# Kernel optimization log

Measured on AMD Instinct MI355X. Metric: run time of the kernel, lower is better.

The kernel has to match this reference:

```python
import jax, jax.numpy as jnp
import numpy as np

H = 12
DH = 64
SCALE = DH ** -0.5

def _ln(x, g, b):
    m = jnp.mean(x, axis=-1, keepdims=True)
    v = jnp.mean((x - m) ** 2, axis=-1, keepdims=True)
    return (x - m) / jnp.sqrt(v + 1e-5) * g + b

def _heads(t):
    b, n, _ = t.shape
    return t.reshape(b, n, H, DH).transpose(0, 2, 1, 3)

def _merge(t):
    b, h, n, d = t.shape
    return t.transpose(0, 2, 1, 3).reshape(b, n, h * d)

def _attn_zero(q, k, v):
    # zero-attn sink: one all-zero K/V token appended -> extra logit exactly 0
    dots = jnp.einsum('bhid,bhjd->bhij', q, k) * SCALE
    dots = jnp.pad(dots, ((0, 0), (0, 0), (0, 0), (0, 1)))
    a = jax.nn.softmax(dots, axis=-1)[..., :-1]  # zero V row contributes nothing
    return jnp.einsum('bhij,bhjd->bhid', a, v)

def _ffn(x, w1, b1, w2, b2):
    return jax.nn.gelu(x @ w1 + b1, approximate=False) @ w2 + b2

def _forward(img, clinic, ln1_g, ln1_b, w_qkv, w_o, b_o, ln2_g, ln2_b,
             w_ff1, b_ff1, w_ff2, b_ff2,
             cn_i_g, cn_i_b, cn_c_g, cn_c_b,
             w_iq, w_ik, w_iv, w_cq, w_ck, w_cv,
             w_io, b_io, w_co, b_co,
             fn_i_g, fn_i_b, fn_c_g, fn_c_b,
             iff_w1, iff_b1, iff_w2, iff_b2,
             cff_w1, cff_b1, cff_w2, cff_b2):
    L = ln1_g.shape[0]
    for l in range(L):  # PreNorm self-attention Transformer stack on image tokens
        xn = _ln(img, ln1_g[l], ln1_b[l])
        q, k, v = jnp.split(xn @ w_qkv[l], 3, axis=-1)
        out = _merge(_attn_zero(_heads(q), _heads(k), _heads(v))) @ w_o[l] + b_o[l]
        img = img + out
        xn = _ln(img, ln2_g[l], ln2_b[l])
        img = img + _ffn(xn, w_ff1[l], b_ff1[l], w_ff2[l], b_ff2[l])
    # Transformer_Cross: dual-stream cross + self attention fusion
    i_n = _ln(img, cn_i_g, cn_i_b)
    c_n = _ln(clinic, cn_c_g, cn_c_b)
    iq, ik, iv = _heads(i_n @ w_iq), _heads(i_n @ w_ik), _heads(i_n @ w_iv)
    cq, ck, cv = _heads(c_n @ w_cq), _heads(c_n @ w_ck), _heads(c_n @ w_cv)
    i_out = (_attn_zero(iq, ck, cv) + _attn_zero(iq, ik, iv)) * 0.5
    c_out = (_attn_zero(cq, ik, iv) + _attn_zero(cq, ck, cv)) * 0.5
    img = img + (_merge(i_out) @ w_io + b_io)
    clinic = clinic + (_merge(c_out) @ w_co + b_co)
    img = img + _ffn(_ln(img, fn_i_g, fn_i_b), iff_w1, iff_b1, iff_w2, iff_b2)
    clinic = clinic + _ffn(_ln(clinic, fn_c_g, fn_c_b), cff_w1, cff_b1, cff_w2, cff_b2)
    return img, clinic

def setup_inputs() -> dict:
    B, NI, NC, D, M, L = 4, 1024, 256, 768, 3072, 2
    INNER = H * DH
    keys = iter(jax.random.split(jax.random.key(0), 48))
    def rn(shape, s=0.02):
        return jax.random.normal(next(keys), shape, jnp.float32) * s
    return {
        'img': jax.random.normal(next(keys), (B, NI, D), jnp.float32),
        'clinic': jax.random.normal(next(keys), (B, NC, D), jnp.float32),
        'ln1_g': jnp.ones((L, D), jnp.float32), 'ln1_b': jnp.zeros((L, D), jnp.float32),
        'w_qkv': rn((L, D, 3 * INNER)), 'w_o': rn((L, INNER, D)), 'b_o': jnp.zeros((L, D), jnp.float32),
        'ln2_g': jnp.ones((L, D), jnp.float32), 'ln2_b': jnp.zeros((L, D), jnp.float32),
        'w_ff1': rn((L, D, M)), 'b_ff1': jnp.zeros((L, M), jnp.float32),
        'w_ff2': rn((L, M, D)), 'b_ff2': jnp.zeros((L, D), jnp.float32),
        'cn_i_g': jnp.ones((D,), jnp.float32), 'cn_i_b': jnp.zeros((D,), jnp.float32),
        'cn_c_g': jnp.ones((D,), jnp.float32), 'cn_c_b': jnp.zeros((D,), jnp.float32),
        'w_iq': rn((D, INNER)), 'w_ik': rn((D, INNER)), 'w_iv': rn((D, INNER)),
        'w_cq': rn((D, INNER)), 'w_ck': rn((D, INNER)), 'w_cv': rn((D, INNER)),
        'w_io': rn((INNER, D)), 'b_io': jnp.zeros((D,), jnp.float32),
        'w_co': rn((INNER, D)), 'b_co': jnp.zeros((D,), jnp.float32),
        'fn_i_g': jnp.ones((D,), jnp.float32), 'fn_i_b': jnp.zeros((D,), jnp.float32),
        'fn_c_g': jnp.ones((D,), jnp.float32), 'fn_c_b': jnp.zeros((D,), jnp.float32),
        'iff_w1': rn((D, M)), 'iff_b1': jnp.zeros((M,), jnp.float32),
        'iff_w2': rn((M, D)), 'iff_b2': jnp.zeros((D,), jnp.float32),
        'cff_w1': rn((D, M)), 'cff_b1': jnp.zeros((M,), jnp.float32),
        'cff_w2': rn((M, D)), 'cff_b2': jnp.zeros((D,), jnp.float32),
    }

def reference(img, clinic, ln1_g, ln1_b, w_qkv, w_o, b_o, ln2_g, ln2_b,
              w_ff1, b_ff1, w_ff2, b_ff2,
              cn_i_g, cn_i_b, cn_c_g, cn_c_b,
              w_iq, w_ik, w_iv, w_cq, w_ck, w_cv,
              w_io, b_io, w_co, b_co,
              fn_i_g, fn_i_b, fn_c_g, fn_c_b,
              iff_w1, iff_b1, iff_w2, iff_b2,
              cff_w1, cff_b1, cff_w2, cff_b2):
    return _forward(img, clinic, ln1_g, ln1_b, w_qkv, w_o, b_o, ln2_g, ln2_b,
                    w_ff1, b_ff1, w_ff2, b_ff2,
                    cn_i_g, cn_i_b, cn_c_g, cn_c_b,
                    w_iq, w_ik, w_iv, w_cq, w_ck, w_cv,
                    w_io, b_io, w_co, b_co,
                    fn_i_g, fn_i_b, fn_c_g, fn_c_b,
                    iff_w1, iff_b1, iff_w2, iff_b2,
                    cff_w1, cff_b1, cff_w2, cff_b2)
```

## Files before the change

kernel.cpp:

```cpp
#include <hip/hip_runtime.h>
#include <stdint.h>
#include <math.h>

typedef unsigned short u16;
typedef short  s16x8 __attribute__((ext_vector_type(8)));
typedef float  f32x4 __attribute__((ext_vector_type(4)));

#define DEVI __device__ __forceinline__

DEVI float b2f(u16 u){ union{unsigned int i; float f;} v; v.i = ((unsigned int)u)<<16; return v.f; }
DEVI u16 f2b(float f){
  union{float f; unsigned int i;} v; v.f = f;
  unsigned int r = v.i + 0x7FFFu + ((v.i >> 16) & 1u);
  return (u16)(r >> 16);
}

template<int MODE, int SPLITK>
__launch_bounds__(256, 2)
__global__ void gemm_bt(const u16* __restrict__ A, const u16* __restrict__ Bt,
                        const float* __restrict__ bias, u16* __restrict__ outb,
                        float* __restrict__ resid, int M, int N, int K)
{
  __shared__ __align__(16) u16 lds_a[128*32];
  __shared__ __align__(16) u16 lds_b[128*32];
  const int tid = threadIdx.x;
  const int w = tid >> 6, l = tid & 63;
  const int q = l >> 4, r = l & 15;
  const int wm = w & 1, wn = w >> 1;
  const size_t m0 = (size_t)blockIdx.y * 128, n0 = (size_t)blockIdx.x * 128;
  const int kslice = K / SPLITK;
  const int kbeg = (SPLITK > 1) ? (int)blockIdx.z * kslice : 0;

  const int srow = tid >> 2;
  const int scol = (tid & 3) * 8;
  const u16* pa0 = A  + (m0 + srow)      * (size_t)K + kbeg + scol;
  const u16* pa1 = A  + (m0 + 64 + srow) * (size_t)K + kbeg + scol;
  const u16* pb0 = Bt + (n0 + srow)      * (size_t)K + kbeg + scol;
  const u16* pb1 = Bt + (n0 + 64 + srow) * (size_t)K + kbeg + scol;

  f32x4 acc[4][4];
  f32x4 zero = {0.f, 0.f, 0.f, 0.f};
#pragma unroll
  for (int i = 0; i < 4; i++)
#pragma unroll
    for (int j = 0; j < 4; j++) acc[i][j] = zero;

  auto compute = [&]() {
    s16x8 af[4], bfr[4];
#pragma unroll
    for (int mm = 0; mm < 4; mm++)
      af[mm] = *(const s16x8*)&lds_a[(wm*64 + mm*16 + r)*32 + q*8];
#pragma unroll
    for (int nn = 0; nn < 4; nn++)
      bfr[nn] = *(const s16x8*)&lds_b[(wn*64 + nn*16 + r)*32 + q*8];
#pragma unroll
    for (int mm = 0; mm < 4; mm++)
#pragma unroll
      for (int nn = 0; nn < 4; nn++)
        acc[mm][nn] = __builtin_amdgcn_mfma_f32_16x16x32_bf16(af[mm], bfr[nn], acc[mm][nn], 0, 0, 0);
  };

  s16x8 a0_0 = *(const s16x8*)(pa0);
  s16x8 a1_0 = *(const s16x8*)(pa1);
  s16x8 b0_0 = *(const s16x8*)(pb0);
  s16x8 b1_0 = *(const s16x8*)(pb1);
  s16x8 a0_1 = *(const s16x8*)(pa0 + 32);
  s16x8 a1_1 = *(const s16x8*)(pa1 + 32);
  s16x8 b0_1 = *(const s16x8*)(pb0 + 32);
  s16x8 b1_1 = *(const s16x8*)(pb1 + 32);

  const int niter = kslice / 32;
  for (int it = 0; it < niter; it += 2){
    __syncthreads();
    *(s16x8*)&lds_a[srow*32 + scol]        = a0_0;
    *(s16x8*)&lds_a[(64 + srow)*32 + scol] = a1_0;
    *(s16x8*)&lds_b[srow*32 + scol]        = b0_0;
    *(s16x8*)&lds_b[(64 + srow)*32 + scol] = b1_0;
    __syncthreads();
    if (it + 2 < niter){
      int k2 = (it + 2) * 32;
      a0_0 = *(const s16x8*)(pa0 + k2);
      a1_0 = *(const s16x8*)(pa1 + k2);
      b0_0 = *(const s16x8*)(pb0 + k2);
      b1_0 = *(const s16x8*)(pb1 + k2);
    }
    compute();
    __syncthreads();
    *(s16x8*)&lds_a[srow*32 + scol]        = a0_1;
    *(s16x8*)&lds_a[(64 + srow)*32 + scol] = a1_1;
    *(s16x8*)&lds_b[srow*32 + scol]        = b0_1;
    *(s16x8*)&lds_b[(64 + srow)*32 + scol] = b1_1;
    __syncthreads();
    if (it + 3 < niter){
      int k3 = (it + 3) * 32;
      a0_1 = *(const s16x8*)(pa0 + k3);
      a1_1 = *(const s16x8*)(pa1 + k3);
      b0_1 = *(const s16x8*)(pb0 + k3);
      b1_1 = *(const s16x8*)(pb1 + k3);
    }
    compute();
  }

#pragma unroll
  for (int nn = 0; nn < 4; nn++){
    size_t col = n0 + wn*64 + nn*16 + r;
    float bv = 0.0f;
    if (MODE != 0 && (SPLITK == 1 || blockIdx.z == 0)) bv = bias[col];
#pragma unroll
    for (int mm = 0; mm < 4; mm++){
#pragma unroll
      for (int j = 0; j < 4; j++){
        size_t row = m0 + wm*64 + mm*16 + q*4 + j;
        float v = acc[mm][nn][j] + bv;
        if (MODE == 1) v = 0.5f * v * (1.0f + erff(v * 0.70710678118654752f));
        if (MODE == 2){
          if (SPLITK > 1) atomicAdd(&resid[row * N + col], v);
          else            resid[row * N + col] += v;
        } else {
          outb[row * N + col] = f2b(v);
        }
      }
    }
  }
}

__launch_bounds__(256, 2)
__global__ void attn_zero_kernel(const u16* __restrict__ Qp, const u16* __restrict__ Kp,
                                 const u16* __restrict__ vT, u16* __restrict__ Op,
                                 int Nq, int Nkv, int LDq, int LDk,
                                 float outw, int accumulate)
{
  __shared__ __align__(16) u16 lds_k[32*64];
  __shared__ __align__(16) u16 lds_v[64*32];
  __shared__ __align__(16) u16 lds_p[4][16*40];

  const int tid = threadIdx.x;
  const int w = tid >> 6, l = tid & 63;
  const int q = l >> 4, r = l & 15;
  const int h = blockIdx.y, b = blockIdx.z;
  const int q0 = blockIdx.x * 64 + w * 16;

  s16x8 qf[2];
  {
    const u16* qrow = Qp + (size_t)(b*Nq + q0 + r) * LDq + h*64;
    qf[0] = *(const s16x8*)(qrow + q*8);
    qf[1] = *(const s16x8*)(qrow + 32 + q*8);
  }

  float m_[4], l_[4];
  f32x4 o[4];
  f32x4 zero = {0.f, 0.f, 0.f, 0.f};
#pragma unroll
  for (int j = 0; j < 4; j++){ m_[j] = 0.0f; l_[j] = 1.0f; }
#pragma unroll
  for (int nn = 0; nn < 4; nn++) o[nn] = zero;

  const u16* Kbase = Kp + (size_t)b * Nkv * LDk + h*64;
  const u16* gk = Kbase + (size_t)(tid >> 3) * LDk + (((tid & 7) ^ ((tid >> 3) & 7)) << 3);
  const u16* Vbase = vT + ((size_t)b * 768 + h*64) * (size_t)Nkv;
  const u16* gv = Vbase + (size_t)(tid >> 2) * Nkv + ((tid & 3) << 3);

  for (int kv0 = 0; kv0 < Nkv; kv0 += 32){
    s16x8 kvv = *(const s16x8*)(gk + (size_t)kv0 * LDk);
    s16x8 vvv = *(const s16x8*)(gv + kv0);
    __syncthreads();
    *(s16x8*)&lds_k[tid * 8] = kvv;
    *(s16x8*)&lds_v[tid * 8] = vvv;
    __syncthreads();

    f32x4 s[2];
#pragma unroll
    for (int kk = 0; kk < 2; kk++){
      int row = kk*16 + r;
      s16x8 kf0 = *(const s16x8*)&lds_k[row*64 + ((q       ^ (row & 7)) << 3)];
      s16x8 kf1 = *(const s16x8*)&lds_k[row*64 + (((4 + q) ^ (row & 7)) << 3)];
      f32x4 t = zero;
      t = __builtin_amdgcn_mfma_f32_16x16x32_bf16(qf[0], kf0, t, 0, 0, 0);
      t = __builtin_amdgcn_mfma_f32_16x16x32_bf16(qf[1], kf1, t, 0, 0, 0);
      s[kk] = t * 0.125f;
    }

    float p0[4], p1[4], al[4];
#pragma unroll
    for (int j = 0; j < 4; j++){
      float mx = fmaxf(s[0][j], s[1][j]);
#pragma unroll
      for (int d = 1; d < 16; d <<= 1) mx = fmaxf(mx, __shfl_xor(mx, d));
      float mn = fmaxf(m_[j], mx);
      float a  = __expf(m_[j] - mn);
      p0[j] = __expf(s[0][j] - mn);
      p1[j] = __expf(s[1][j] - mn);
      float rs = p0[j] + p1[j];
#pragma unroll
      for (int d = 1; d < 16; d <<= 1) rs += __shfl_xor(rs, d);
      l_[j] = l_[j] * a + rs;
      m_[j] = mn; al[j] = a;
    }
#pragma unroll
    for (int nn = 0; nn < 4; nn++){
      f32x4 t = o[nn];
#pragma unroll
      for (int j = 0; j < 4; j++) t[j] *= al[j];
      o[nn] = t;
    }

    u16* P = &lds_p[w][0];
#pragma unroll
    for (int j = 0; j < 4; j++){
      P[(q*4 + j)*40 + r]      = f2b(p0[j]);
      P[(q*4 + j)*40 + 16 + r] = f2b(p1[j]);
    }
    s16x8 pf = *(const s16x8*)&P[r*40 + q*8];
#pragma unroll
    for (int nn = 0; nn < 4; nn++){
      int row = nn*16 + r;
      s16x8 vf = *(const s16x8*)&lds_v[row*32 + (q << 3)];
      o[nn] = __builtin_amdgcn_mfma_f32_16x16x32_bf16(pf, vf, o[nn], 0, 0, 0);
    }
  }

#pragma unroll
  for (int j = 0; j < 4; j++){
    float inv = outw / l_[j];
    size_t rowoff = (size_t)(b*Nq + q0 + q*4 + j) * 768 + h*64;
#pragma unroll
    for (int nn = 0; nn < 4; nn++){
      float v = o[nn][j] * inv;
      size_t idx = rowoff + nn*16 + r;
      if (accumulate) v += b2f(Op[idx]);
      Op[idx] = f2b(v);
    }
  }
}

__launch_bounds__(256)
__global__ void ln_kernel(const float* __restrict__ x, const float* __restrict__ g,
                          const float* __restrict__ bta, u16* __restrict__ out)
{
  __shared__ float red[8];
  const size_t row = blockIdx.x;
  const float* xr = x + row * 768;
  int t = threadIdx.x;
  float v0 = xr[t], v1 = xr[t + 256], v2 = xr[t + 512];
  float s  = v0 + v1 + v2;
  float s2 = v0*v0 + v1*v1 + v2*v2;
#pragma unroll
  for (int d = 1; d < 64; d <<= 1){ s += __shfl_xor(s, d); s2 += __shfl_xor(s2, d); }
  int w = t >> 6;
  if ((t & 63) == 0){ red[w] = s; red[4 + w] = s2; }
  __syncthreads();
  s  = red[0] + red[1] + red[2] + red[3];
  s2 = red[4] + red[5] + red[6] + red[7];
  float mean = s * (1.0f / 768.0f);
  float var  = s2 * (1.0f / 768.0f) - mean * mean;
  float rstd = rsqrtf(var + 1e-5f);
  u16* orow = out + row * 768;
  orow[t]       = f2b((v0 - mean) * rstd * g[t]       + bta[t]);
  orow[t + 256] = f2b((v1 - mean) * rstd * g[t + 256] + bta[t + 256]);
  orow[t + 512] = f2b((v2 - mean) * rstd * g[t + 512] + bta[t + 512]);
}

__global__ void transpose_kernel(const float* __restrict__ in, u16* __restrict__ out, int R, int C)
{
  __shared__ u16 tile[64][65];
  int c0 = blockIdx.x * 64, r0 = blockIdx.y * 64;
  for (int i = threadIdx.y; i < 64; i += 4)
    tile[i][threadIdx.x] = f2b(in[(size_t)(r0 + i) * C + c0 + threadIdx.x]);
  __syncthreads();
  for (int i = threadIdx.y; i < 64; i += 4)
    out[(size_t)(c0 + i) * R + r0 + threadIdx.x] = tile[threadIdx.x][i];
}

__global__ void transpose_v_kernel(const u16* __restrict__ in, u16* __restrict__ out,
                                   int N, int LD, int coff)
{
  __shared__ u16 tile[64][65];
  int bz = blockIdx.z;
  int c0 = blockIdx.x * 64, n0 = blockIdx.y * 64;
  const u16* ib = in + ((size_t)bz * N + n0) * LD + coff + c0;
  for (int i = threadIdx.y; i < 64; i += 4)
    tile[i][threadIdx.x] = ib[(size_t)i * LD + threadIdx.x];
  __syncthreads();
  u16* ob = out + ((size_t)bz * 768 + c0) * N + n0;
  for (int i = threadIdx.y; i < 64; i += 4)
    ob[(size_t)i * N + threadIdx.x] = tile[threadIdx.x][i];
}

__global__ void copy_f32(const float* __restrict__ in, float* __restrict__ out, long n4){
  long i = (long)blockIdx.x * blockDim.x + threadIdx.x;
  long stride = (long)gridDim.x * blockDim.x;
  const f32x4* in4 = (const f32x4*)in;
  f32x4* out4 = (f32x4*)out;
  for (; i < n4; i += stride) out4[i] = in4[i];
}

extern "C" void kernel_launch(void* const* d_in, const int* in_sizes, int n_in,
                              void* d_out, int out_size, void* d_ws, size_t ws_size,
                              hipStream_t stream)
{
  const int B = 4, NI = 1024, NC = 256, D = 768, FF = 3072, H = 12, L = 2;
  const int RI = B * NI;
  const int RC = B * NC;

  const float* img    = (const float*)d_in[0];
  const float* clinic = (const float*)d_in[1];
  const float* ln1_g  = (const float*)d_in[2];
  const float* ln1_b  = (const float*)d_in[3];
  const float* w_qkv  = (const float*)d_in[4];
  const float* w_o    = (const float*)d_in[5];
  const float* b_o    = (const float*)d_in[6];
  const float* ln2_g  = (const float*)d_in[7];
  const float* ln2_b  = (const float*)d_in[8];
  const float* w_ff1  = (const float*)d_in[9];
  const float* b_ff1  = (const float*)d_in[10];
  const float* w_ff2  = (const float*)d_in[11];
  const float* b_ff2  = (const float*)d_in[12];
  const float* cn_i_g = (const float*)d_in[13];
  const float* cn_i_b = (const float*)d_in[14];
  const float* cn_c_g = (const float*)d_in[15];
  const float* cn_c_b = (const float*)d_in[16];
  const float* w_iq   = (const float*)d_in[17];
  const float* w_ik   = (const float*)d_in[18];
  const float* w_iv   = (const float*)d_in[19];
  const float* w_cq   = (const float*)d_in[20];
  const float* w_ck   = (const float*)d_in[21];
  const float* w_cv   = (const float*)d_in[22];
  const float* w_io   = (const float*)d_in[23];
  const float* b_io   = (const float*)d_in[24];
  const float* w_co   = (const float*)d_in[25];
  const float* b_co   = (const float*)d_in[26];
  const float* fn_i_g = (const float*)d_in[27];
  const float* fn_i_b = (const float*)d_in[28];
  const float* fn_c_g = (const float*)d_in[29];
  const float* fn_c_b = (const float*)d_in[30];
  const float* iff_w1 = (const float*)d_in[31];
  const float* iff_b1 = (const float*)d_in[32];
  const float* iff_w2 = (const float*)d_in[33];
  const float* iff_b2 = (const float*)d_in[34];
  const float* cff_w1 = (const float*)d_in[35];
  const float* cff_b1 = (const float*)d_in[36];
  const float* cff_w2 = (const float*)d_in[37];
  const float* cff_b2 = (const float*)d_in[38];

  char* ws = (char*)d_ws;
  size_t off = 0;
  auto alloc = [&](size_t elems, size_t esz) -> void* {
    void* p = ws + off;
    off += ((elems * esz) + 255) & ~(size_t)255;
    return p;
  };
  u16* wqkvT[2]; u16* woT[2]; u16* ff1T[2]; u16* ff2T[2];
  for (int i = 0; i < 2; i++) wqkvT[i] = (u16*)alloc((size_t)3*D*D, 2);
  for (int i = 0; i < 2; i++) woT[i]   = (u16*)alloc((size_t)D*D, 2);
  for (int i = 0; i < 2; i++) ff1T[i]  = (u16*)alloc((size_t)FF*D, 2);
  for (int i = 0; i < 2; i++) ff2T[i]  = (u16*)alloc((size_t)D*FF, 2);
  u16* wiqkvT = (u16*)alloc((size_t)3*D*D, 2);
  u16* wcqkvT = (u16*)alloc((size_t)3*D*D, 2);
  u16* wioT = (u16*)alloc((size_t)D*D, 2); u16* wcoT = (u16*)alloc((size_t)D*D, 2);
  u16* iff1T = (u16*)alloc((size_t)FF*D, 2); u16* iff2T = (u16*)alloc((size_t)D*FF, 2);
  u16* cff1T = (u16*)alloc((size_t)FF*D, 2); u16* cff2T = (u16*)alloc((size_t)D*FF, 2);

  float* img_f = (float*)alloc((size_t)RI*D, 4);
  float* cli_f = (float*)alloc((size_t)RC*D, 4);
  u16* xn_i = (u16*)alloc((size_t)RI*D, 2);
  u16* xn_c = (u16*)alloc((size_t)RC*D, 2);
  u16* region = (u16*)alloc((size_t)RI*FF, 2);
  u16* qkvb = region;
  u16* cqkv = region + (size_t)RI*3*D;
  u16* h1   = region;
  u16* ao_i = (u16*)alloc((size_t)RI*D, 2);
  u16* ao_c = (u16*)alloc((size_t)RC*D, 2);
  u16* vT_i = (u16*)alloc((size_t)B*D*NI, 2);
  u16* vT_c = (u16*)alloc((size_t)B*D*NC, 2);
  (void)ws_size; (void)in_sizes; (void)n_in; (void)out_size;

  auto T = [&](const float* in_, u16* out_, int R, int C){
    transpose_kernel<<<dim3(C/64, R/64), dim3(64, 4), 0, stream>>>(in_, out_, R, C);
  };
  auto TV = [&](const u16* in_, u16* out_, int N, int LD, int coff){
    transpose_v_kernel<<<dim3(D/64, N/64, B), dim3(64, 4), 0, stream>>>(in_, out_, N, LD, coff);
  };
  auto G0 = [&](const u16* A, const u16* Bt, u16* out_, int M, int N, int K){
    gemm_bt<0,1><<<dim3(N/128, M/128), 256, 0, stream>>>(A, Bt, nullptr, out_, nullptr, M, N, K);
  };
  auto G1 = [&](const u16* A, const u16* Bt, const float* bias, u16* out_, int M, int N, int K){
    gemm_bt<1,1><<<dim3(N/128, M/128), 256, 0, stream>>>(A, Bt, bias, out_, nullptr, M, N, K);
  };
  auto G2 = [&](const u16* A, const u16* Bt, const float* bias, float* resid, int M, int N, int K, int splitk){
    if (splitk == 4)
      gemm_bt<2,4><<<dim3(N/128, M/128, 4), 256, 0, stream>>>(A, Bt, bias, nullptr, resid, M, N, K);
    else if (splitk == 2)
      gemm_bt<2,2><<<dim3(N/128, M/128, 2), 256, 0, stream>>>(A, Bt, bias, nullptr, resid, M, N, K);
    else
      gemm_bt<2,1><<<dim3(N/128, M/128, 1), 256, 0, stream>>>(A, Bt, bias, nullptr, resid, M, N, K);
  };
  auto ATT = [&](const u16* Q, const u16* K_, const u16* vTp, u16* O,
                 int Nq, int Nkv, int LDq, int LDk, float w_, int acc_){
    attn_zero_kernel<<<dim3(Nq/64, H, B), 256, 0, stream>>>(Q, K_, vTp, O, Nq, Nkv, LDq, LDk, w_, acc_);
  };
  auto CP = [&](const float* in_, float* out_, long n){
    copy_f32<<<1024, 256, 0, stream>>>(in_, out_, n / 4);
  };

  for (int li = 0; li < L; li++){
    T(w_qkv + (size_t)li*D*3*D, wqkvT[li], D, 3*D);
    T(w_o   + (size_t)li*D*D,   woT[li],   D, D);
    T(w_ff1 + (size_t)li*D*FF,  ff1T[li],  D, FF);
    T(w_ff2 + (size_t)li*FF*D,  ff2T[li],  FF, D);
  }
  T(w_iq, wiqkvT,              D, D);
  T(w_ik, wiqkvT + (size_t)D*D,   D, D);
  T(w_iv, wiqkvT + (size_t)2*D*D, D, D);
  T(w_cq, wcqkvT,              D, D);
  T(w_ck, wcqkvT + (size_t)D*D,   D, D);
  T(w_cv, wcqkvT + (size_t)2*D*D, D, D);
  T(w_io, wioT, D, D); T(w_co, wcoT, D, D);
  T(iff_w1, iff1T, D, FF); T(iff_w2, iff2T, FF, D);
  T(cff_w1, cff1T, D, FF); T(cff_w2, cff2T, FF, D);

  CP(img,    img_f, (long)RI*D);
  CP(clinic, cli_f, (long)RC*D);

  for (int li = 0; li < L; li++){
    ln_kernel<<<RI, 256, 0, stream>>>(img_f, ln1_g + li*D, ln1_b + li*D, xn_i);
    G0(xn_i, wqkvT[li], qkvb, RI, 3*D, D);
    TV(qkvb, vT_i, NI, 3*D, 2*D);
    ATT(qkvb, qkvb + D, vT_i, ao_i, NI, NI, 3*D, 3*D, 1.0f, 0);
    G2(ao_i, woT[li], b_o + li*D, img_f, RI, D, D, 2);
    ln_kernel<<<RI, 256, 0, stream>>>(img_f, ln2_g + li*D, ln2_b + li*D, xn_i);
    G1(xn_i, ff1T[li], b_ff1 + li*FF, h1, RI, FF, D);
    G2(h1, ff2T[li], b_ff2 + li*D, img_f, RI, D, FF, 2);
  }

  ln_kernel<<<RI, 256, 0, stream>>>(img_f, cn_i_g, cn_i_b, xn_i);
  ln_kernel<<<RC, 256, 0, stream>>>(cli_f, cn_c_g, cn_c_b, xn_c);
  u16* iqkv = qkvb;
  u16* cqk  = cqkv;
  G0(xn_i, wiqkvT, iqkv, RI, 3*D, D);
  G0(xn_c, wcqkvT, cqk,  RC, 3*D, D);
  TV(iqkv, vT_i, NI, 3*D, 2*D);
  TV(cqk,  vT_c, NC, 3*D, 2*D);

  ATT(iqkv, cqk + D,  vT_c, ao_i, NI, NC, 3*D, 3*D, 0.5f, 0);
  ATT(iqkv, iqkv + D, vT_i, ao_i, NI, NI, 3*D, 3*D, 0.5f, 1);
  ATT(cqk,  iqkv + D, vT_i, ao_c, NC, NI, 3*D, 3*D, 0.5f, 0);
  ATT(cqk,  cqk + D,  vT_c, ao_c, NC, NC, 3*D, 3*D, 0.5f, 1);

  G2(ao_i, wioT, b_io, img_f, RI, D, D, 2);
  G2(ao_c, wcoT, b_co, cli_f, RC, D, D, 4);

  ln_kernel<<<RI, 256, 0, stream>>>(img_f, fn_i_g, fn_i_b, xn_i);
  G1(xn_i, iff1T, iff_b1, h1, RI, FF, D);
  G2(h1, iff2T, iff_b2, img_f, RI, D, FF, 2);

  ln_kernel<<<RC, 256, 0, stream>>>(cli_f, fn_c_g, fn_c_b, xn_c);
  G1(xn_c, cff1T, cff_b1, h1, RC, FF, D);
  G2(h1, cff2T, cff_b2, cli_f, RC, D, FF, 4);

  CP(img_f, (float*)d_out,                (long)RI*D);
  CP(cli_f, (float*)d_out + (size_t)RI*D, (long)RC*D);
}
```

Baseline: 1.109 ms.

## Load GEMM tiles directly to LDS and prefetch next K/V tile in attention

The GEMM main loop drops its register double-buffered prefetch and instead issues global_load_lds 16-byte direct-to-LDS loads each K step, with a single-stage loop bracketed by barriers. This removes the register staging and LDS write instructions, but loses overlap of the next tile's global load with the current MFMA work, so load latency is now exposed every iteration. The attention kernel gains a one-tile register prefetch of K and V so the next block's global loads are in flight while the current block is computed.

```diff
diff --git a/kernel.cpp b/kernel.cpp
--- a/kernel.cpp
+++ b/kernel.cpp
@@ -13,6 +13,12 @@
   union{float f; unsigned int i;} v; v.f = f;
   unsigned int r = v.i + 0x7FFFu + ((v.i >> 16) & 1u);
   return (u16)(r >> 16);
+}
+
+typedef __attribute__((address_space(1))) const unsigned int as1_uint;
+typedef __attribute__((address_space(3))) unsigned int as3_uint;
+DEVI void gload16(const void* g, void* l){
+  __builtin_amdgcn_global_load_lds((as1_uint*)g, (as3_uint*)l, 16, 0, 0);
 }
 
 template<int MODE, int SPLITK>
@@ -37,6 +43,10 @@
   const u16* pa1 = A  + (m0 + 64 + srow) * (size_t)K + kbeg + scol;
   const u16* pb0 = Bt + (n0 + srow)      * (size_t)K + kbeg + scol;
   const u16* pb1 = Bt + (n0 + 64 + srow) * (size_t)K + kbeg + scol;
+  u16* la0 = &lds_a[srow*32 + scol];
+  u16* la1 = &lds_a[(64 + srow)*32 + scol];
+  u16* lb0 = &lds_b[srow*32 + scol];
+  u16* lb1 = &lds_b[(64 + srow)*32 + scol];
 
   f32x4 acc[4][4];
   f32x4 zero = {0.f, 0.f, 0.f, 0.f};
@@ -45,7 +55,16 @@
 #pragma unroll
     for (int j = 0; j < 4; j++) acc[i][j] = zero;
 
-  auto compute = [&]() {
+  const int niter = kslice / 32;
+  for (int it = 0; it < niter; ++it){
+    const size_t koff = (size_t)it * 32;
+    __syncthreads();
+    gload16(pa0 + koff, la0);
+    gload16(pa1 + koff, la1);
+    gload16(pb0 + koff, lb0);
+    gload16(pb1 + koff, lb1);
+    __syncthreads();
+
     s16x8 af[4], bfr[4];
 #pragma unroll
     for (int mm = 0; mm < 4; mm++)
@@ -58,47 +77,6 @@
 #pragma unroll
       for (int nn = 0; nn < 4; nn++)
         acc[mm][nn] = __builtin_amdgcn_mfma_f32_16x16x32_bf16(af[mm], bfr[nn], acc[mm][nn], 0, 0, 0);
-  };
-
-  s16x8 a0_0 = *(const s16x8*)(pa0);
-  s16x8 a1_0 = *(const s16x8*)(pa1);
-  s16x8 b0_0 = *(const s16x8*)(pb0);
-  s16x8 b1_0 = *(const s16x8*)(pb1);
-  s16x8 a0_1 = *(const s16x8*)(pa0 + 32);
-  s16x8 a1_1 = *(const s16x8*)(pa1 + 32);
-  s16x8 b0_1 = *(const s16x8*)(pb0 + 32);
-  s16x8 b1_1 = *(const s16x8*)(pb1 + 32);
-
-  const int niter = kslice / 32;
-  for (int it = 0; it < niter; it += 2){
-    __syncthreads();
-    *(s16x8*)&lds_a[srow*32 + scol]        = a0_0;
-    *(s16x8*)&lds_a[(64 + srow)*32 + scol] = a1_0;
-    *(s16x8*)&lds_b[srow*32 + scol]        = b0_0;
-    *(s16x8*)&lds_b[(64 + srow)*32 + scol] = b1_0;
-    __syncthreads();
-    if (it + 2 < niter){
-      int k2 = (it + 2) * 32;
-      a0_0 = *(const s16x8*)(pa0 + k2);
-      a1_0 = *(const s16x8*)(pa1 + k2);
-      b0_0 = *(const s16x8*)(pb0 + k2);
-      b1_0 = *(const s16x8*)(pb1 + k2);
-    }
-    compute();
-    __syncthreads();
-    *(s16x8*)&lds_a[srow*32 + scol]        = a0_1;
-    *(s16x8*)&lds_a[(64 + srow)*32 + scol] = a1_1;
-    *(s16x8*)&lds_b[srow*32 + scol]        = b0_1;
-    *(s16x8*)&lds_b[(64 + srow)*32 + scol] = b1_1;
-    __syncthreads();
-    if (it + 3 < niter){
-      int k3 = (it + 3) * 32;
-      a0_1 = *(const s16x8*)(pa0 + k3);
-      a1_1 = *(const s16x8*)(pa1 + k3);
-      b0_1 = *(const s16x8*)(pb0 + k3);
-      b1_1 = *(const s16x8*)(pb1 + k3);
-    }
-    compute();
   }
 
 #pragma unroll
@@ -160,13 +138,18 @@
   const u16* Vbase = vT + ((size_t)b * 768 + h*64) * (size_t)Nkv;
   const u16* gv = Vbase + (size_t)(tid >> 2) * Nkv + ((tid & 3) << 3);
 
+  s16x8 kvv = *(const s16x8*)(gk);
+  s16x8 vvv = *(const s16x8*)(gv);
+
   for (int kv0 = 0; kv0 < Nkv; kv0 += 32){
-    s16x8 kvv = *(const s16x8*)(gk + (size_t)kv0 * LDk);
-    s16x8 vvv = *(const s16x8*)(gv + kv0);
     __syncthreads();
     *(s16x8*)&lds_k[tid * 8] = kvv;
     *(s16x8*)&lds_v[tid * 8] = vvv;
     __syncthreads();
+    if (kv0 + 32 < Nkv){
+      kvv = *(const s16x8*)(gk + (size_t)(kv0 + 32) * LDk);
+      vvv = *(const s16x8*)(gv + (kv0 + 32));
+    }
 
     f32x4 s[2];
 #pragma unroll
```

Result: slower. 1.131 ms (+2.0%).

## Double KV tile to 64 and prefetch next tile into registers in attention

Applied to the files above, without the earlier changes.

The zero-sink attention kernel now processes 64 KV tokens per iteration instead of 32. It loads the next tile's K and V into registers while computing the current one, so global loads overlap with MFMA and softmax work. The V tile is now stored XOR-swizzled to avoid LDS bank conflicts, and P is written in two 16x32 halves. This halves the number of barriers and online-softmax rescales, at the cost of more LDS, more registers, and the assumption that Nkv is a multiple of 64.

```diff
diff --git a/kernel.cpp b/kernel.cpp
--- a/kernel.cpp
+++ b/kernel.cpp
@@ -130,9 +130,9 @@
                                  int Nq, int Nkv, int LDq, int LDk,
                                  float outw, int accumulate)
 {
-  __shared__ __align__(16) u16 lds_k[32*64];
-  __shared__ __align__(16) u16 lds_v[64*32];
-  __shared__ __align__(16) u16 lds_p[4][16*40];
+  __shared__ __align__(16) u16 lds_k[64*64];
+  __shared__ __align__(16) u16 lds_v[64*64];
+  __shared__ __align__(16) u16 lds_p[4][2][16*40];
 
   const int tid = threadIdx.x;
   const int w = tid >> 6, l = tid & 63;
@@ -155,22 +155,38 @@
 #pragma unroll
   for (int nn = 0; nn < 4; nn++) o[nn] = zero;
 
+  const int crow = tid >> 3;
+  const int ccol = ((tid & 7) ^ (crow & 7)) << 3;
   const u16* Kbase = Kp + (size_t)b * Nkv * LDk + h*64;
-  const u16* gk = Kbase + (size_t)(tid >> 3) * LDk + (((tid & 7) ^ ((tid >> 3) & 7)) << 3);
+  const u16* gk = Kbase + (size_t)crow * LDk + ccol;
   const u16* Vbase = vT + ((size_t)b * 768 + h*64) * (size_t)Nkv;
-  const u16* gv = Vbase + (size_t)(tid >> 2) * Nkv + ((tid & 3) << 3);
-
-  for (int kv0 = 0; kv0 < Nkv; kv0 += 32){
-    s16x8 kvv = *(const s16x8*)(gk + (size_t)kv0 * LDk);
-    s16x8 vvv = *(const s16x8*)(gv + kv0);
-    __syncthreads();
-    *(s16x8*)&lds_k[tid * 8] = kvv;
-    *(s16x8*)&lds_v[tid * 8] = vvv;
-    __syncthreads();
-
-    f32x4 s[2];
-#pragma unroll
-    for (int kk = 0; kk < 2; kk++){
+  const u16* gv = Vbase + (size_t)crow * Nkv + ccol;
+  const size_t gk32 = (size_t)32 * LDk;
+  const size_t gv32 = (size_t)32 * Nkv;
+
+  s16x8 kr0 = *(const s16x8*)(gk);
+  s16x8 kr1 = *(const s16x8*)(gk + gk32);
+  s16x8 vr0 = *(const s16x8*)(gv);
+  s16x8 vr1 = *(const s16x8*)(gv + gv32);
+
+  for (int kv0 = 0; kv0 < Nkv; kv0 += 64){
+    __syncthreads();
+    *(s16x8*)&lds_k[tid * 8]         = kr0;
+    *(s16x8*)&lds_k[(256 + tid) * 8] = kr1;
+    *(s16x8*)&lds_v[tid * 8]         = vr0;
+    *(s16x8*)&lds_v[(256 + tid) * 8] = vr1;
+    __syncthreads();
+    if (kv0 + 64 < Nkv){
+      const u16* gkn = gk + (size_t)(kv0 + 64) * LDk;
+      kr0 = *(const s16x8*)(gkn);
+      kr1 = *(const s16x8*)(gkn + gk32);
+      vr0 = *(const s16x8*)(gv + (kv0 + 64));
+      vr1 = *(const s16x8*)(gv + (kv0 + 64) + gv32);
+    }
+
+    f32x4 s[4];
+#pragma unroll
+    for (int kk = 0; kk < 4; kk++){
       int row = kk*16 + r;
       s16x8 kf0 = *(const s16x8*)&lds_k[row*64 + ((q       ^ (row & 7)) << 3)];
       s16x8 kf1 = *(const s16x8*)&lds_k[row*64 + (((4 + q) ^ (row & 7)) << 3)];
@@ -180,17 +196,19 @@
       s[kk] = t * 0.125f;
     }
 
-    float p0[4], p1[4], al[4];
+    float p0[4], p1[4], p2[4], p3[4], al[4];
 #pragma unroll
     for (int j = 0; j < 4; j++){
-      float mx = fmaxf(s[0][j], s[1][j]);
+      float mx = fmaxf(fmaxf(s[0][j], s[1][j]), fmaxf(s[2][j], s[3][j]));
 #pragma unroll
       for (int d = 1; d < 16; d <<= 1) mx = fmaxf(mx, __shfl_xor(mx, d));
       float mn = fmaxf(m_[j], mx);
       float a  = __expf(m_[j] - mn);
       p0[j] = __expf(s[0][j] - mn);
       p1[j] = __expf(s[1][j] - mn);
-      float rs = p0[j] + p1[j];
+      p2[j] = __expf(s[2][j] - mn);
+      p3[j] = __expf(s[3][j] - mn);
+      float rs = (p0[j] + p1[j]) + (p2[j] + p3[j]);
 #pragma unroll
       for (int d = 1; d < 16; d <<= 1) rs += __shfl_xor(rs, d);
       l_[j] = l_[j] * a + rs;
@@ -204,18 +222,24 @@
       o[nn] = t;
     }
 
-    u16* P = &lds_p[w][0];
+    u16* P0 = &lds_p[w][0][0];
+    u16* P1 = &lds_p[w][1][0];
 #pragma unroll
     for (int j = 0; j < 4; j++){
-      P[(q*4 + j)*40 + r]      = f2b(p0[j]);
-      P[(q*4 + j)*40 + 16 + r] = f2b(p1[j]);
-    }
-    s16x8 pf = *(const s16x8*)&P[r*40 + q*8];
+      P0[(q*4 + j)*40 + r]      = f2b(p0[j]);
+      P0[(q*4 + j)*40 + 16 + r] = f2b(p1[j]);
+      P1[(q*4 + j)*40 + r]      = f2b(p2[j]);
+      P1[(q*4 + j)*40 + 16 + r] = f2b(p3[j]);
+    }
+    s16x8 pf0 = *(const s16x8*)&P0[r*40 + q*8];
+    s16x8 pf1 = *(const s16x8*)&P1[r*40 + q*8];
 #pragma unroll
     for (int nn = 0; nn < 4; nn++){
       int row = nn*16 + r;
-      s16x8 vf = *(const s16x8*)&lds_v[row*32 + (q << 3)];
-      o[nn] = __builtin_amdgcn_mfma_f32_16x16x32_bf16(pf, vf, o[nn], 0, 0, 0);
+      s16x8 vf0 = *(const s16x8*)&lds_v[row*64 + ((q       ^ (row & 7)) << 3)];
+      s16x8 vf1 = *(const s16x8*)&lds_v[row*64 + (((4 + q) ^ (row & 7)) << 3)];
+      o[nn] = __builtin_amdgcn_mfma_f32_16x16x32_bf16(pf0, vf0, o[nn], 0, 0, 0);
+      o[nn] = __builtin_amdgcn_mfma_f32_16x16x32_bf16(pf1, vf1, o[nn], 0, 0, 0);
     }
   }
 
```

Measured after the change: 1.001 ms. -9.7%, faster.
